# Optimization experiments

Measured on AMD Instinct MI355X. Metric: run time of the kernel, lower is better.

## Reference

```python
import jax, jax.numpy as jnp
import numpy as np

N_NODES = 50000
N_EDGES = 1600000
N_FEAT = 128
DROPOUT = 0.1


def setup_inputs() -> dict:
    key = jax.random.key(0)
    k1, k2, k3, k4 = jax.random.split(key, 4)
    x = jax.random.normal(k1, (N_NODES, N_FEAT), dtype=jnp.float32)
    adj_vals = jax.random.uniform(k2, (N_EDGES,), dtype=jnp.float32)
    row = jax.random.randint(k3, (N_EDGES,), 0, N_NODES, dtype=jnp.int32)
    col = jax.random.randint(k4, (N_EDGES,), 0, N_NODES, dtype=jnp.int32)
    return {"x": x, "adj_vals": adj_vals, "row": row, "col": col}


def reference(x, adj_vals, row, col):
    # MixedDropout on sparse adjacency values (deterministic fixed key),
    # then SpMM: out[i] = sum_{e: row[e]==i} A_drop[e] * x[col[e]]
    keep_prob = 1.0 - DROPOUT
    mask_key = jax.random.fold_in(jax.random.key(42), 7)
    keep = jax.random.bernoulli(mask_key, keep_prob, adj_vals.shape)
    vals_drop = jnp.where(keep, adj_vals / keep_prob, 0.0)
    # gather source features and weight by (dropped) edge values
    msgs = vals_drop[:, None] * x[col]  # [E, F]
    out = jax.ops.segment_sum(msgs, row, num_segments=N_NODES)  # [N, F]
    return out
```

## Files before the change

kernel.cpp:

```cpp
#include <hip/hip_runtime.h>
#include <stdint.h>

#define N_NODES 50000
#define N_EDGES 1600000
#define N_FEAT 128
#define CAP 64
#define OVF_CAP 65536

#define RSHIFT 8
#define BROWS 256
#define NB 196
#define NWG_A 256
#define A_THREADS 1024
#define CAPW 56
#define EPW (N_EDGES / NWG_A)


struct KeyPair { uint32_t a, b; };

__host__ __device__ constexpr inline uint32_t rotl32(uint32_t x, int r) {
  return (x << r) | (x >> (32 - r));
}

__host__ __device__ constexpr inline KeyPair threefry2x32(uint32_t k0, uint32_t k1,
                                                          uint32_t x0, uint32_t x1) {
  const uint32_t ks0 = k0, ks1 = k1, ks2 = k0 ^ k1 ^ 0x1BD11BDAu;
  x0 += ks0;
  x1 += ks1;
  const int rotA[4] = {13, 15, 26, 6};
  const int rotB[4] = {17, 29, 16, 24};
  const uint32_t ks[3] = {ks0, ks1, ks2};
  for (int i = 0; i < 5; ++i) {
    const int* rot = (i & 1) ? rotB : rotA;
    for (int j = 0; j < 4; ++j) {
      x0 += x1;
      x1 = rotl32(x1, rot[j]);
      x1 ^= x0;
    }
    x0 += ks[(i + 1) % 3];
    x1 += ks[(i + 2) % 3] + (uint32_t)(i + 1);
  }
  return {x0, x1};
}

constexpr KeyPair MASK_KEY = threefry2x32(0u, 42u, 0u, 7u);

__device__ inline bool edge_keep(uint32_t e) {
  KeyPair r = threefry2x32(MASK_KEY.a, MASK_KEY.b, 0u, e);
  uint32_t bits = r.a ^ r.b;
  float u = __uint_as_float((bits >> 9) | 0x3f800000u) - 1.0f;
  return u < 0.9f;
}

__device__ inline uint32_t f2bf(uint32_t b) {
  return (b + 0x7fffu + ((b >> 16) & 1u)) >> 16;
}


__global__ void __launch_bounds__(A_THREADS) convA_kernel(const float* __restrict__ x,
                                                          uint32_t* __restrict__ xb,
                                                          const float* __restrict__ adj_vals,
                                                          const int* __restrict__ row,
                                                          const int* __restrict__ col,
                                                          uint64_t* __restrict__ coarse,
                                                          uint32_t* __restrict__ lens,
                                                          uint32_t* __restrict__ ovf_count,
                                                          uint64_t* __restrict__ ovf) {
  __shared__ uint32_t cnt[NB];
  int wg = blockIdx.x;
  int tid = threadIdx.x;
  if (tid < NB) cnt[tid] = 0;

  const int gthreads = NWG_A * A_THREADS;
  for (int i = wg * A_THREADS + tid; i < (N_NODES * N_FEAT) / 4; i += gthreads) {
    float4 f = ((const float4*)x)[i];
    uint2 o;
    o.x = f2bf(__float_as_uint(f.x)) | (f2bf(__float_as_uint(f.y)) << 16);
    o.y = f2bf(__float_as_uint(f.z)) | (f2bf(__float_as_uint(f.w)) << 16);
    ((uint2*)xb)[i] = o;
  }
  __syncthreads();

  int e0 = wg * EPW;
  int e1 = e0 + EPW;
  for (int e = e0 + tid; e < e1; e += A_THREADS) {
    if (!edge_keep((uint32_t)e)) continue;
    float v = adj_vals[e] / 0.9f;
    uint32_t r = (uint32_t)row[e];
    uint32_t c = (uint32_t)col[e];
    uint32_t b = r >> RSHIFT;
    uint32_t li = atomicAdd(&cnt[b], 1u);
    uint64_t p = ((uint64_t)r << 48) | ((uint64_t)c << 32) | (uint64_t)__float_as_uint(v);
    if (li < CAPW) {
      coarse[((size_t)b * NWG_A + wg) * CAPW + li] = p;
    } else {
      uint32_t oi = atomicAdd(ovf_count, 1u);
      if (oi < OVF_CAP) ovf[oi] = p;
    }
  }
  __syncthreads();
  if (tid < NB) lens[(size_t)tid * NWG_A + wg] = min(cnt[tid], (uint32_t)CAPW);
}

__global__ void __launch_bounds__(1024) partB_kernel(const uint64_t* __restrict__ coarse,
                                                     const uint32_t* __restrict__ lens,
                                                     uint32_t* __restrict__ payload,
                                                     uint32_t* __restrict__ cursor,
                                                     uint32_t* __restrict__ ovf_count,
                                                     uint64_t* __restrict__ ovf) {
  int b = blockIdx.x;
  int tid = threadIdx.x;
  __shared__ uint32_t s[NWG_A];
  __shared__ uint32_t cnt[BROWS];
  if (tid < NWG_A) s[tid] = lens[(size_t)b * NWG_A + tid];
  if (tid < BROWS) cnt[tid] = 0;
  __syncthreads();
  for (int off = 1; off < NWG_A; off <<= 1) {
    uint32_t v = 0, u = 0;
    if (tid < NWG_A) {
      v = s[tid];
      u = (tid >= off) ? s[tid - off] : 0u;
    }
    __syncthreads();
    if (tid < NWG_A) s[tid] = v + u;
    __syncthreads();
  }
  int seg = tid >> 2;
  int sub = tid & 3;
  uint32_t sbase = (seg == 0) ? 0u : s[seg - 1];
  uint32_t slen = s[seg] - sbase;
  const uint64_t* cseg = coarse + ((size_t)b * NWG_A + seg) * CAPW;
  for (uint32_t li = (uint32_t)sub; li < slen; li += 4) {
    uint64_t p = cseg[li];
    uint32_t r = (uint32_t)(p >> 48);
    uint32_t rl = r & (BROWS - 1);
    uint32_t idx = atomicAdd(&cnt[rl], 1u);
    if (idx < CAP) {
      uint32_t c = (uint32_t)(p >> 32) & 0xFFFFu;
      payload[(size_t)r * CAP + idx] = (c << 16) | f2bf((uint32_t)p);
    } else {
      uint32_t oi = atomicAdd(ovf_count, 1u);
      if (oi < OVF_CAP) ovf[oi] = p;
    }
  }
  __syncthreads();
  for (int k = tid; k < BROWS; k += 1024) {
    uint32_t r = ((uint32_t)b << RSHIFT) + (uint32_t)k;
    if (r < N_NODES) {
      uint32_t c0 = min(cnt[k], (uint32_t)CAP);
      cursor[r] = r * CAP + c0;
      uint32_t np = min((c0 + 7u) & ~7u, (uint32_t)CAP);
      for (uint32_t i2 = c0; i2 < np; ++i2) payload[(size_t)r * CAP + i2] = 0u;
    }
  }
}

typedef float f4v __attribute__((ext_vector_type(4)));

__global__ void __launch_bounds__(256) gather_bf16_kernel(const uint32_t* __restrict__ xb,
                                                          const uint32_t* __restrict__ payload,
                                                          const uint32_t* __restrict__ cursor,
                                                          float* __restrict__ out) {
  int r = blockIdx.x * 16 + (threadIdx.x >> 4);
  int lane = threadIdx.x & 15;
  uint32_t base = (uint32_t)r * CAP;
  uint32_t cnt = cursor[r] - base;
  uint32_t n = (cnt + 7u) & ~7u;
  const uint4* x4 = (const uint4*)xb;

  float acc0 = 0.f, acc1 = 0.f, acc2 = 0.f, acc3 = 0.f;
  float acc4 = 0.f, acc5 = 0.f, acc6 = 0.f, acc7 = 0.f;

  uint32_t p0 = __builtin_nontemporal_load(payload + base + lane);
  uint32_t p1 = __builtin_nontemporal_load(payload + base + 16 + lane);
  uint32_t p2 = (n > 32u) ? __builtin_nontemporal_load(payload + base + 32 + lane) : 0u;
  uint32_t p3 = (n > 48u) ? __builtin_nontemporal_load(payload + base + 48 + lane) : 0u;

#define GSTEP(ww)                                                            \
  {                                                                          \
    uint32_t cc = (ww) >> 16;                                                \
    float vv = __uint_as_float((ww) << 16);                                  \
    uint4 a = x4[(size_t)cc * 16 + lane];                                    \
    acc0 += vv * __uint_as_float(a.x << 16);                                 \
    acc1 += vv * __uint_as_float(a.x & 0xffff0000u);                         \
    acc2 += vv * __uint_as_float(a.y << 16);                                 \
    acc3 += vv * __uint_as_float(a.y & 0xffff0000u);                         \
    acc4 += vv * __uint_as_float(a.z << 16);                                 \
    acc5 += vv * __uint_as_float(a.z & 0xffff0000u);                         \
    acc6 += vv * __uint_as_float(a.w << 16);                                 \
    acc7 += vv * __uint_as_float(a.w & 0xffff0000u);                         \
  }

#define PCHUNK(preg, mm)                                                     \
  for (int j = 0; j < (mm); j += 8) {                                        \
    uint32_t w0 = __shfl((preg), j + 0, 16);                                 \
    uint32_t w1 = __shfl((preg), j + 1, 16);                                 \
    uint32_t w2 = __shfl((preg), j + 2, 16);                                 \
    uint32_t w3 = __shfl((preg), j + 3, 16);                                 \
    uint32_t w4 = __shfl((preg), j + 4, 16);                                 \
    uint32_t w5 = __shfl((preg), j + 5, 16);                                 \
    uint32_t w6 = __shfl((preg), j + 6, 16);                                 \
    uint32_t w7 = __shfl((preg), j + 7, 16);                                 \
    GSTEP(w0) GSTEP(w1) GSTEP(w2) GSTEP(w3)                                  \
    GSTEP(w4) GSTEP(w5) GSTEP(w6) GSTEP(w7)                                  \
  }

  int rem = (int)n;
  PCHUNK(p0, min(rem, 16));
  rem -= 16;
  if (rem > 0) {
    PCHUNK(p1, min(rem, 16));
    rem -= 16;
    if (rem > 0) {
      PCHUNK(p2, min(rem, 16));
      rem -= 16;
      if (rem > 0) {
        PCHUNK(p3, min(rem, 16));
      }
    }
  }
#undef PCHUNK
#undef GSTEP

  f4v lo, hi;
  lo.x = acc0; lo.y = acc1; lo.z = acc2; lo.w = acc3;
  hi.x = acc4; hi.y = acc5; hi.z = acc6; hi.w = acc7;
  f4v* o = (f4v*)out + (size_t)r * 32 + lane * 2;
  __builtin_nontemporal_store(lo, o);
  __builtin_nontemporal_store(hi, o + 1);
}

__global__ void __launch_bounds__(256) ovf_pack_kernel(const float* __restrict__ x,
                                                       const uint32_t* __restrict__ ovf_count,
                                                       const uint64_t* __restrict__ ovf,
                                                       float* __restrict__ out) {
  uint32_t n = *ovf_count;
  if (n > OVF_CAP) n = OVF_CAP;
  int g = (int)((blockIdx.x * blockDim.x + threadIdx.x) >> 7);
  int f = threadIdx.x & 127;
  const int ngroups = (64 * 256) >> 7;
  for (uint32_t oi = g; oi < n; oi += ngroups) {
    uint64_t p = ovf[oi];
    uint32_t r = (uint32_t)(p >> 48);
    uint32_t c = (uint32_t)((p >> 32) & 0xFFFFu);
    float v = __uint_as_float((uint32_t)p);
    atomicAdd(&out[(size_t)r * N_FEAT + f], v * x[(size_t)c * N_FEAT + f]);
  }
}


__global__ void __launch_bounds__(256) scatter_fused_kernel(const float* __restrict__ x,
                                                            const float* __restrict__ adj_vals,
                                                            const int* __restrict__ row,
                                                            const int* __restrict__ col,
                                                            float* __restrict__ out) {
  long long t = (long long)blockIdx.x * blockDim.x + threadIdx.x;
  int e = (int)(t >> 6);
  int lane = (int)(t & 63);
  if (e >= N_EDGES) return;
  if (!edge_keep((uint32_t)e)) return;
  float v = adj_vals[e] / 0.9f;
  float2 xf = *(const float2*)(x + (long long)col[e] * N_FEAT + lane * 2);
  float* dst = out + (long long)row[e] * N_FEAT + lane * 2;
  atomicAdd(dst, v * xf.x);
  atomicAdd(dst + 1, v * xf.y);
}


extern "C" void kernel_launch(void* const* d_in, const int* in_sizes, int n_in,
                              void* d_out, int out_size, void* d_ws, size_t ws_size,
                              hipStream_t stream) {
  const float* x        = (const float*)d_in[0];
  const float* adj_vals = (const float*)d_in[1];
  const int*   row      = (const int*)d_in[2];
  const int*   col      = (const int*)d_in[3];
  float* out = (float*)d_out;

  size_t a_cursor  = 0;
  size_t a_ovfc    = (a_cursor + (size_t)N_NODES * 4 + 255) & ~255ull;
  size_t a_ovf     = (a_ovfc + 4 + 255) & ~255ull;
  size_t a_lens    = (a_ovf + (size_t)OVF_CAP * 8 + 255) & ~255ull;
  size_t a_coarse  = (a_lens + (size_t)NB * NWG_A * 4 + 255) & ~255ull;
  size_t a_payload = (a_coarse + (size_t)NB * NWG_A * CAPW * 8 + 255) & ~255ull;
  size_t a_xb      = (a_payload + (size_t)N_NODES * CAP * 4 + 255) & ~255ull;
  size_t need      = a_xb + (size_t)N_NODES * N_FEAT * 2;

  if (ws_size >= need) {
    uint32_t* cursor    = (uint32_t*)((char*)d_ws + a_cursor);
    uint32_t* ovf_count = (uint32_t*)((char*)d_ws + a_ovfc);
    uint64_t* ovf       = (uint64_t*)((char*)d_ws + a_ovf);
    uint32_t* lens      = (uint32_t*)((char*)d_ws + a_lens);
    uint64_t* coarse    = (uint64_t*)((char*)d_ws + a_coarse);
    uint32_t* payload   = (uint32_t*)((char*)d_ws + a_payload);
    uint32_t* xb        = (uint32_t*)((char*)d_ws + a_xb);

    hipMemsetAsync(ovf_count, 0, 4, stream);
    convA_kernel<<<NWG_A, A_THREADS, 0, stream>>>(x, xb, adj_vals, row, col,
                                                  coarse, lens, ovf_count, ovf);
    partB_kernel<<<NB, 1024, 0, stream>>>(coarse, lens, payload, cursor, ovf_count, ovf);
    gather_bf16_kernel<<<N_NODES / 16, 256, 0, stream>>>(xb, payload, cursor, out);
    ovf_pack_kernel<<<64, 256, 0, stream>>>(x, ovf_count, ovf, out);
  } else {
    hipMemsetAsync(d_out, 0, (size_t)out_size * sizeof(float), stream);
    long long total_threads = (long long)N_EDGES * 64;
    scatter_fused_kernel<<<(int)((total_threads + 255) / 256), 256, 0, stream>>>(
        x, adj_vals, row, col, out);
  }
}
```

Baseline: 162.9 us.

## Replace two-pass binned CSR build with single-pass global-atomic row binning

Removes the coarse bucket buffer and the second partitioning kernel, so each kept edge directly atomically increments a global per-row cursor and writes its packed column/value word into the row's payload slot. The cursor array is now zeroed with a memset and holds raw counts. The gather kernel clamps the count to CAP and masks out trailing lanes instead of relying on zero-padded payload slots. This trades one kernel launch and an intermediate round trip through memory for about 1.44M global atomics with random addresses, plus atomicExch stores.

```diff
diff --git a/kernel.cpp b/kernel.cpp
--- a/kernel.cpp
+++ b/kernel.cpp
@@ -7,13 +7,7 @@
 #define CAP 64
 #define OVF_CAP 65536
 
-#define RSHIFT 8
-#define BROWS 256
-#define NB 196
-#define NWG_A 256
-#define A_THREADS 1024
-#define CAPW 56
-#define EPW (N_EDGES / NWG_A)
+#define CONV_BLOCKS 1600
 
 
 struct KeyPair { uint32_t a, b; };
@@ -56,101 +50,49 @@
   return (b + 0x7fffu + ((b >> 16) & 1u)) >> 16;
 }
 
-
-__global__ void __launch_bounds__(A_THREADS) convA_kernel(const float* __restrict__ x,
-                                                          uint32_t* __restrict__ xb,
-                                                          const float* __restrict__ adj_vals,
-                                                          const int* __restrict__ row,
-                                                          const int* __restrict__ col,
-                                                          uint64_t* __restrict__ coarse,
-                                                          uint32_t* __restrict__ lens,
-                                                          uint32_t* __restrict__ ovf_count,
-                                                          uint64_t* __restrict__ ovf) {
-  __shared__ uint32_t cnt[NB];
-  int wg = blockIdx.x;
-  int tid = threadIdx.x;
-  if (tid < NB) cnt[tid] = 0;
-
-  const int gthreads = NWG_A * A_THREADS;
-  for (int i = wg * A_THREADS + tid; i < (N_NODES * N_FEAT) / 4; i += gthreads) {
+__global__ void __launch_bounds__(256) convbin_kernel(const float* __restrict__ x,
+                                                      uint32_t* __restrict__ xb,
+                                                      const float* __restrict__ adj_vals,
+                                                      const int* __restrict__ row,
+                                                      const int* __restrict__ col,
+                                                      uint32_t* __restrict__ payload,
+                                                      uint32_t* __restrict__ cursor,
+                                                      uint32_t* __restrict__ ovf_count,
+                                                      uint64_t* __restrict__ ovf) {
+  const int t = blockIdx.x * 256 + threadIdx.x;
+  const int T = CONV_BLOCKS * 256;
+
+  for (int i = t; i < (N_NODES * N_FEAT) / 4; i += T) {
     float4 f = ((const float4*)x)[i];
     uint2 o;
     o.x = f2bf(__float_as_uint(f.x)) | (f2bf(__float_as_uint(f.y)) << 16);
     o.y = f2bf(__float_as_uint(f.z)) | (f2bf(__float_as_uint(f.w)) << 16);
     ((uint2*)xb)[i] = o;
   }
-  __syncthreads();
-
-  int e0 = wg * EPW;
-  int e1 = e0 + EPW;
-  for (int e = e0 + tid; e < e1; e += A_THREADS) {
-    if (!edge_keep((uint32_t)e)) continue;
-    float v = adj_vals[e] / 0.9f;
-    uint32_t r = (uint32_t)row[e];
-    uint32_t c = (uint32_t)col[e];
-    uint32_t b = r >> RSHIFT;
-    uint32_t li = atomicAdd(&cnt[b], 1u);
-    uint64_t p = ((uint64_t)r << 48) | ((uint64_t)c << 32) | (uint64_t)__float_as_uint(v);
-    if (li < CAPW) {
-      coarse[((size_t)b * NWG_A + wg) * CAPW + li] = p;
+
+  const int e4 = t * 4;
+  if (e4 >= N_EDGES) return;
+  const int4 r4 = ((const int4*)row)[t];
+  const int4 c4 = ((const int4*)col)[t];
+  const float4 a4 = ((const float4*)adj_vals)[t];
+  const int rr[4] = {r4.x, r4.y, r4.z, r4.w};
+  const int cc[4] = {c4.x, c4.y, c4.z, c4.w};
+  const float aa[4] = {a4.x, a4.y, a4.z, a4.w};
+#pragma unroll
+  for (int k = 0; k < 4; ++k) {
+    const uint32_t e = (uint32_t)(e4 + k);
+    if (!edge_keep(e)) continue;
+    const uint32_t r = (uint32_t)rr[k];
+    const uint32_t c = (uint32_t)cc[k];
+    const float v = aa[k] / 0.9f;
+    const uint32_t idx = atomicAdd(&cursor[r], 1u);
+    if (idx < CAP) {
+      const uint32_t w = (c << 16) | f2bf(__float_as_uint(v));
+      atomicExch(&payload[(size_t)r * CAP + idx], w);
     } else {
-      uint32_t oi = atomicAdd(ovf_count, 1u);
-      if (oi < OVF_CAP) ovf[oi] = p;
-    }
-  }
-  __syncthreads();
-  if (tid < NB) lens[(size_t)tid * NWG_A + wg] = min(cnt[tid], (uint32_t)CAPW);
-}
-
-__global__ void __launch_bounds__(1024) partB_kernel(const uint64_t* __restrict__ coarse,
-                                                     const uint32_t* __restrict__ lens,
-                                                     uint32_t* __restrict__ payload,
-                                                     uint32_t* __restrict__ cursor,
-                                                     uint32_t* __restrict__ ovf_count,
-                                                     uint64_t* __restrict__ ovf) {
-  int b = blockIdx.x;
-  int tid = threadIdx.x;
-  __shared__ uint32_t s[NWG_A];
-  __shared__ uint32_t cnt[BROWS];
-  if (tid < NWG_A) s[tid] = lens[(size_t)b * NWG_A + tid];
-  if (tid < BROWS) cnt[tid] = 0;
-  __syncthreads();
-  for (int off = 1; off < NWG_A; off <<= 1) {
-    uint32_t v = 0, u = 0;
-    if (tid < NWG_A) {
-      v = s[tid];
-      u = (tid >= off) ? s[tid - off] : 0u;
-    }
-    __syncthreads();
-    if (tid < NWG_A) s[tid] = v + u;
-    __syncthreads();
-  }
-  int seg = tid >> 2;
-  int sub = tid & 3;
-  uint32_t sbase = (seg == 0) ? 0u : s[seg - 1];
-  uint32_t slen = s[seg] - sbase;
-  const uint64_t* cseg = coarse + ((size_t)b * NWG_A + seg) * CAPW;
-  for (uint32_t li = (uint32_t)sub; li < slen; li += 4) {
-    uint64_t p = cseg[li];
-    uint32_t r = (uint32_t)(p >> 48);
-    uint32_t rl = r & (BROWS - 1);
-    uint32_t idx = atomicAdd(&cnt[rl], 1u);
-    if (idx < CAP) {
-      uint32_t c = (uint32_t)(p >> 32) & 0xFFFFu;
-      payload[(size_t)r * CAP + idx] = (c << 16) | f2bf((uint32_t)p);
-    } else {
-      uint32_t oi = atomicAdd(ovf_count, 1u);
-      if (oi < OVF_CAP) ovf[oi] = p;
-    }
-  }
-  __syncthreads();
-  for (int k = tid; k < BROWS; k += 1024) {
-    uint32_t r = ((uint32_t)b << RSHIFT) + (uint32_t)k;
-    if (r < N_NODES) {
-      uint32_t c0 = min(cnt[k], (uint32_t)CAP);
-      cursor[r] = r * CAP + c0;
-      uint32_t np = min((c0 + 7u) & ~7u, (uint32_t)CAP);
-      for (uint32_t i2 = c0; i2 < np; ++i2) payload[(size_t)r * CAP + i2] = 0u;
+      const uint32_t oi = atomicAdd(ovf_count, 1u);
+      if (oi < OVF_CAP)
+        ovf[oi] = ((uint64_t)r << 48) | ((uint64_t)c << 32) | (uint64_t)__float_as_uint(v);
     }
   }
 }
@@ -164,17 +106,17 @@
   int r = blockIdx.x * 16 + (threadIdx.x >> 4);
   int lane = threadIdx.x & 15;
   uint32_t base = (uint32_t)r * CAP;
-  uint32_t cnt = cursor[r] - base;
-  uint32_t n = (cnt + 7u) & ~7u;
+  uint32_t cnt = cursor[r];
+  if (cnt > CAP) cnt = CAP;
   const uint4* x4 = (const uint4*)xb;
 
   float acc0 = 0.f, acc1 = 0.f, acc2 = 0.f, acc3 = 0.f;
   float acc4 = 0.f, acc5 = 0.f, acc6 = 0.f, acc7 = 0.f;
 
   uint32_t p0 = __builtin_nontemporal_load(payload + base + lane);
-  uint32_t p1 = __builtin_nontemporal_load(payload + base + 16 + lane);
-  uint32_t p2 = (n > 32u) ? __builtin_nontemporal_load(payload + base + 32 + lane) : 0u;
-  uint32_t p3 = (n > 48u) ? __builtin_nontemporal_load(payload + base + 48 + lane) : 0u;
+  uint32_t p1 = (cnt > 16u) ? __builtin_nontemporal_load(payload + base + 16 + lane) : 0u;
+  uint32_t p2 = (cnt > 32u) ? __builtin_nontemporal_load(payload + base + 32 + lane) : 0u;
+  uint32_t p3 = (cnt > 48u) ? __builtin_nontemporal_load(payload + base + 48 + lane) : 0u;
 
 #define GSTEP(ww)                                                            \
   {                                                                          \
@@ -193,6 +135,7 @@
 
 #define PCHUNK(preg, mm)                                                     \
   for (int j = 0; j < (mm); j += 8) {                                        \
+    int lim = (mm) - j;                                                      \
     uint32_t w0 = __shfl((preg), j + 0, 16);                                 \
     uint32_t w1 = __shfl((preg), j + 1, 16);                                 \
     uint32_t w2 = __shfl((preg), j + 2, 16);                                 \
@@ -201,21 +144,30 @@
     uint32_t w5 = __shfl((preg), j + 5, 16);                                 \
     uint32_t w6 = __shfl((preg), j + 6, 16);                                 \
     uint32_t w7 = __shfl((preg), j + 7, 16);                                 \
+    w1 = (1 < lim) ? w1 : 0u;                                                \
+    w2 = (2 < lim) ? w2 : 0u;                                                \
+    w3 = (3 < lim) ? w3 : 0u;                                                \
+    w4 = (4 < lim) ? w4 : 0u;                                                \
+    w5 = (5 < lim) ? w5 : 0u;                                                \
+    w6 = (6 < lim) ? w6 : 0u;                                                \
+    w7 = (7 < lim) ? w7 : 0u;                                                \
     GSTEP(w0) GSTEP(w1) GSTEP(w2) GSTEP(w3)                                  \
     GSTEP(w4) GSTEP(w5) GSTEP(w6) GSTEP(w7)                                  \
   }
 
-  int rem = (int)n;
-  PCHUNK(p0, min(rem, 16));
-  rem -= 16;
+  int rem = (int)cnt;
   if (rem > 0) {
-    PCHUNK(p1, min(rem, 16));
+    PCHUNK(p0, min(rem, 16));
     rem -= 16;
     if (rem > 0) {
-      PCHUNK(p2, min(rem, 16));
+      PCHUNK(p1, min(rem, 16));
       rem -= 16;
       if (rem > 0) {
-        PCHUNK(p3, min(rem, 16));
+        PCHUNK(p2, min(rem, 16));
+        rem -= 16;
+        if (rem > 0) {
+          PCHUNK(p3, min(rem, 16));
+        }
       }
     }
   }
@@ -277,11 +229,9 @@
   float* out = (float*)d_out;
 
   size_t a_cursor  = 0;
-  size_t a_ovfc    = (a_cursor + (size_t)N_NODES * 4 + 255) & ~255ull;
+  size_t a_ovfc    = (size_t)N_NODES * 4;
   size_t a_ovf     = (a_ovfc + 4 + 255) & ~255ull;
-  size_t a_lens    = (a_ovf + (size_t)OVF_CAP * 8 + 255) & ~255ull;
-  size_t a_coarse  = (a_lens + (size_t)NB * NWG_A * 4 + 255) & ~255ull;
-  size_t a_payload = (a_coarse + (size_t)NB * NWG_A * CAPW * 8 + 255) & ~255ull;
+  size_t a_payload = (a_ovf + (size_t)OVF_CAP * 8 + 255) & ~255ull;
   size_t a_xb      = (a_payload + (size_t)N_NODES * CAP * 4 + 255) & ~255ull;
   size_t need      = a_xb + (size_t)N_NODES * N_FEAT * 2;
 
@@ -289,15 +239,12 @@
     uint32_t* cursor    = (uint32_t*)((char*)d_ws + a_cursor);
     uint32_t* ovf_count = (uint32_t*)((char*)d_ws + a_ovfc);
     uint64_t* ovf       = (uint64_t*)((char*)d_ws + a_ovf);
-    uint32_t* lens      = (uint32_t*)((char*)d_ws + a_lens);
-    uint64_t* coarse    = (uint64_t*)((char*)d_ws + a_coarse);
     uint32_t* payload   = (uint32_t*)((char*)d_ws + a_payload);
     uint32_t* xb        = (uint32_t*)((char*)d_ws + a_xb);
 
-    hipMemsetAsync(ovf_count, 0, 4, stream);
-    convA_kernel<<<NWG_A, A_THREADS, 0, stream>>>(x, xb, adj_vals, row, col,
-                                                  coarse, lens, ovf_count, ovf);
-    partB_kernel<<<NB, 1024, 0, stream>>>(coarse, lens, payload, cursor, ovf_count, ovf);
+    hipMemsetAsync(d_ws, 0, (size_t)N_NODES * 4 + 4, stream);
+    convbin_kernel<<<CONV_BLOCKS, 256, 0, stream>>>(x, xb, adj_vals, row, col,
+                                                    payload, cursor, ovf_count, ovf);
     gather_bf16_kernel<<<N_NODES / 16, 256, 0, stream>>>(xb, payload, cursor, out);
     ovf_pack_kernel<<<64, 256, 0, stream>>>(x, ovf_count, ovf, out);
   } else {
```

Result: slower. 265.8 us (+63.1%).
